# Optimization experiments

Measured on AMD Instinct MI355X. Metric: run time of the kernel, lower is better.

The kernel has to match this reference:

```python
import jax, jax.numpy as jnp
import numpy as np
import math

B, S, D, H, DFF, V = 8, 512, 512, 8, 2048, 32000
EPS = 1e-5

def _pe_table(max_len, d):
    pos = jnp.arange(max_len, dtype=jnp.float32)[:, None]
    i = jnp.arange(d)
    exponent = (2 * (i // 2)).astype(jnp.float32) / d
    angle = pos / jnp.power(10000.0, exponent)[None, :]
    return jnp.where(i % 2 == 0, jnp.sin(angle), jnp.cos(angle))

def _ln(x, g, b):
    mu = jnp.mean(x, -1, keepdims=True)
    var = jnp.mean((x - mu) ** 2, -1, keepdims=True)
    return g * (x - mu) * jax.lax.rsqrt(var + EPS) + b

def setup_inputs() -> dict:
    key = jax.random.key(0)
    ks = jax.random.split(key, 16)
    n = jax.random.normal
    return {
        "tokens": jax.random.randint(ks[0], (B, S), 0, V, dtype=jnp.int32),
        "emb": n(ks[1], (V, D), jnp.float32),
        "pe": _pe_table(1000, D),
        "Wq": n(ks[2], (H, D, D), jnp.float32), "bq": jnp.zeros((H, D), jnp.float32),
        "Wk": n(ks[3], (H, D, D), jnp.float32), "bk": jnp.zeros((H, D), jnp.float32),
        "Wv": n(ks[4], (H, D, D), jnp.float32), "bv": jnp.zeros((H, D), jnp.float32),
        "Wo": n(ks[5], (H * D, D), jnp.float32), "bo": jnp.zeros((D,), jnp.float32),
        "g1": jnp.ones((D,), jnp.float32), "be1": jnp.zeros((D,), jnp.float32),
        "W1": n(ks[6], (D, DFF), jnp.float32), "b1": jnp.zeros((DFF,), jnp.float32),
        "W2": n(ks[7], (DFF, D), jnp.float32), "b2": jnp.zeros((D,), jnp.float32),
        "g2": jnp.ones((D,), jnp.float32), "be2": jnp.zeros((D,), jnp.float32),
        "Wf": n(ks[8], (D, V), jnp.float32), "bf": jnp.zeros((V,), jnp.float32),
    }

def reference(tokens, emb, pe, Wq, bq, Wk, bk, Wv, bv, Wo, bo, g1, be1,
              W1, b1, W2, b2, g2, be2, Wf, bf):
    x = emb[tokens] + pe[:tokens.shape[1]]  # [B,S,D]
    res = x
    # input-level "causal" mask over (seq, feature) plane, as in the source
    mask = jnp.triu(jnp.ones((S, D), dtype=bool), k=1)
    xm = jnp.where(mask, 0.0, x)
    scale = 1.0 / math.sqrt(D)
    q = jnp.einsum('bsd,hde->hbse', xm, Wq) + bq[:, None, None, :]
    k = jnp.einsum('bsd,hde->hbse', xm, Wk) + bk[:, None, None, :]
    v = jnp.einsum('bsd,hde->hbse', xm, Wv) + bv[:, None, None, :]
    attn = jax.nn.softmax(jnp.einsum('hbse,hbte->hbst', q, k) * scale, axis=-1)
    o = jnp.einsum('hbst,hbte->hbse', attn, v)  # [H,B,S,D]
    cat = o.transpose(1, 2, 0, 3).reshape(B, S, H * D)  # matches torch.cat head order
    x = _ln(res + (cat @ Wo + bo), g1, be1)
    res = x
    ff = jax.nn.relu(x @ W1 + b1) @ W2 + b2
    x = _ln(res + ff, g2, be2)
    return x @ Wf + bf  # [B,S,V]
```

## Files before the change

### kernel.cpp

```cpp
#include <hip/hip_runtime.h>

typedef unsigned short u16;
typedef unsigned int u32;
typedef short s16x8 __attribute__((ext_vector_type(8)));
typedef __bf16 bf16x8 __attribute__((ext_vector_type(8)));
typedef float f32x4 __attribute__((ext_vector_type(4)));

#define DEVI static __device__ __forceinline__

#define SS 512
#define DD 512
#define NFF 2048
#define VV 32000
#define MTOT 4096
#define HD 4096
#define KC 1536

DEVI float bf2f(u16 h){ return __uint_as_float(((u32)h) << 16); }
DEVI u16 f2bf(float f){
  u32 u = __float_as_uint(f);
  return (u16)((u + 0x7FFFu + ((u >> 16) & 1u)) >> 16);
}
DEVI float ldf(const void* p, long i, int isbf){
  return isbf ? bf2f(((const u16*)p)[i]) : ((const float*)p)[i];
}

DEVI f32x4 mfma16(s16x8 a, s16x8 b, f32x4 c){
  return __builtin_amdgcn_mfma_f32_16x16x32_bf16(
      __builtin_bit_cast(bf16x8, a), __builtin_bit_cast(bf16x8, b), c, 0, 0, 0);
}

typedef const __attribute__((address_space(1))) unsigned int* gup;
typedef __attribute__((address_space(3))) unsigned int* lup;
DEVI void gload16(const void* g, void* l){
  __builtin_amdgcn_global_load_lds((gup)g, (lup)l, 16, 0, 0);
}

DEVI float wave_redsum(float v){
  #pragma unroll
  for (int off = 32; off > 0; off >>= 1) v += __shfl_xor(v, off, 64);
  return v;
}

__global__ void k_dflag(const void* pe, int* flag){
  flag[0] = (*(const u32*)pe == 0x3F800000u) ? 1 : 0;
}

__global__ __launch_bounds__(256) void k_embed(
    const int* __restrict__ tok, const void* __restrict__ emb, const void* __restrict__ pe,
    float* __restrict__ x, u16* __restrict__ xm2, const int* __restrict__ dflag)
{
  int isbf = dflag[0];
  int blk = blockIdx.x;
  int s = blk & (SS - 1);
  int t = tok[blk];
  long rb = (long)blk * 1024;
  for (int d = threadIdx.x; d < DD; d += 256){
    float e = ldf(emb, (long)t * DD + d, isbf) + ldf(pe, (long)s * DD + d, isbf);
    x[(long)blk * DD + d] = e;
    float m = (d <= s) ? e : 0.f;
    u16 hi = f2bf(m);
    u16 lo = f2bf(m - bf2f(hi));
    xm2[rb + d] = hi;
    xm2[rb + 512 + d] = lo;
  }
}

__global__ __launch_bounds__(256) void k_wsplitT(
    const void* __restrict__ Wq, const void* __restrict__ Wk,
    u16* __restrict__ Wq2, u16* __restrict__ Wk2, const int* __restrict__ dflag)
{
  int isbf = dflag[0];
  int zz = blockIdx.z;
  const void* in = (zz < 8) ? Wq : Wk;
  u16* out = (zz < 8) ? Wq2 : Wk2;
  int z = zz & 7;
  long zin = (long)z * DD * DD;
  long zout = (long)z * DD * 1024;
  __shared__ float t[32][33];
  int e0 = blockIdx.x * 32, d0 = blockIdx.y * 32;
  int tx = threadIdx.x & 31, ty = threadIdx.x >> 5;
  #pragma unroll
  for (int i = 0; i < 4; i++){
    int d = ty + i * 8;
    t[d][tx] = ldf(in, zin + (long)(d0 + d) * DD + e0 + tx, isbf);
  }
  __syncthreads();
  #pragma unroll
  for (int i = 0; i < 4; i++){
    int e = ty + i * 8;
    float v = t[tx][e];
    u16 hi = f2bf(v);
    u16 lo = f2bf(v - bf2f(hi));
    long ob = zout + (long)(e0 + e) * 1024 + d0 + tx;
    out[ob] = hi;
    out[ob + 512] = lo;
  }
}

__global__ __launch_bounds__(256) void k_transAll(
    const void* __restrict__ Wv, const void* __restrict__ Wo,
    const void* __restrict__ W1, const void* __restrict__ W2,
    const void* __restrict__ Wf,
    u16* __restrict__ WvT, u16* __restrict__ WoT, u16* __restrict__ W1T,
    u16* __restrict__ W2T, u16* __restrict__ WfT, const int* __restrict__ dflag)
{
  int isbf = dflag[0];
  int f = blockIdx.x;
  const void* in; u16* out; int R, C, gx, loc;
  if (f < 2048)      { in = Wv; out = WvT; R = 512;  C = 512;   gx = 16;   loc = f; }
  else if (f < 4096) { in = Wo; out = WoT; R = 4096; C = 512;   gx = 16;   loc = f - 2048; }
  else if (f < 5120) { in = W1; out = W1T; R = 512;  C = 2048;  gx = 64;   loc = f - 4096; }
  else if (f < 6144) { in = W2; out = W2T; R = 2048; C = 512;   gx = 16;   loc = f - 5120; }
  else               { in = Wf; out = WfT; R = 512;  C = 32000; gx = 1000; loc = f - 6144; }
  int bx = loc % gx;
  int rest = loc / gx;
  int gy = R >> 5;
  int by = rest % gy, z = rest / gy;
  long zo = (long)z * R * C;
  __shared__ float t[32][33];
  int c0 = bx * 32, r0 = by * 32;
  int tx = threadIdx.x & 31, ty = threadIdx.x >> 5;
  #pragma unroll
  for (int i = 0; i < 4; i++){
    int r = ty + i * 8;
    t[r][tx] = ldf(in, zo + (long)(r0 + r) * C + c0 + tx, isbf);
  }
  __syncthreads();
  #pragma unroll
  for (int i = 0; i < 4; i++){
    int c = ty + i * 8;
    out[zo + (long)(c0 + c) * R + r0 + tx] = f2bf(t[tx][c]);
  }
}

enum { EP_QK = 0, EP_SCALE = 1, EP_VT = 2, EP_CAT = 3, EP_OUT = 4,
       EP_F32RES = 5, EP_RELU = 6 };

template<int MODE, bool GSWAP>
__global__ __launch_bounds__(256) void k_mfma(
    const u16* __restrict__ A, long sA, int lda,
    const u16* __restrict__ Bt, long sB,
    void* __restrict__ Cv,
    const void* __restrict__ bias,
    const float* __restrict__ res,
    int K, int ldc, float scale,
    const int* __restrict__ dflag)
{
  int isbf = dflag[0];
  int z = blockIdx.z;
  const u16* Ab = A + (long)z * sA;
  const u16* Bb = Bt + (long)z * sB;
  __shared__ __align__(16) u16 As[2][4][128][8];
  __shared__ __align__(16) u16 Bs[2][4][128][8];
  int m0 = (GSWAP ? blockIdx.x : blockIdx.y) * 128;
  int n0 = (GSWAP ? blockIdx.y : blockIdx.x) * 128;
  int tid = threadIdx.x;
  int lane = tid & 63, w = tid >> 6;
  int wr = (w >> 1) * 64, wc = (w & 1) * 64;
  int l15 = lane & 15, l4 = lane >> 4;
  int s0 = w * 64 + lane;
  int ar0 = s0 & 127, ak0 = s0 >> 7;
  int ak1 = ak0 + 2;
  f32x4 zero = {0.f, 0.f, 0.f, 0.f};
  f32x4 acc[4][4];
  #pragma unroll
  for (int i = 0; i < 4; i++)
    #pragma unroll
    for (int j = 0; j < 4; j++) acc[i][j] = zero;

  const long arow0 = (long)(m0 + ar0) * lda;
  const long brow0 = (long)(n0 + ar0) * K;

  #define STAGE(buf, k0) do{ \
    u16* AsF = &As[buf][0][0][0]; \
    u16* BsF = &Bs[buf][0][0][0]; \
    gload16(Ab + arow0 + (k0) + ak0 * 8, AsF + (long)(w * 64) * 8); \
    gload16(Ab + arow0 + (k0) + ak1 * 8, AsF + (long)(256 + w * 64) * 8); \
    gload16(Bb + brow0 + (k0) + ak0 * 8, BsF + (long)(w * 64) * 8); \
    gload16(Bb + brow0 + (k0) + ak1 * 8, BsF + (long)(256 + w * 64) * 8); \
  }while(0)

  #define COMPUTE(buf) do{ \
    s16x8 af[4], bfr[4]; \
    _Pragma("unroll") \
    for (int i = 0; i < 4; i++) af[i] = *(const s16x8*)&As[buf][l4][wr + i * 16 + l15][0]; \
    _Pragma("unroll") \
    for (int j = 0; j < 4; j++) bfr[j] = *(const s16x8*)&Bs[buf][l4][wc + j * 16 + l15][0]; \
    _Pragma("unroll") \
    for (int i = 0; i < 4; i++) \
      _Pragma("unroll") \
      for (int j = 0; j < 4; j++) \
        acc[i][j] = mfma16(af[i], bfr[j], acc[i][j]); \
  }while(0)

  STAGE(0, 0);
  __syncthreads();
  for (int k0 = 0; k0 < K; k0 += 64){
    STAGE(1, k0 + 32);
    COMPUTE(0);
    __syncthreads();
    if (k0 + 64 < K) STAGE(0, k0 + 64);
    COMPUTE(1);
    __syncthreads();
  }
  #undef STAGE
  #undef COMPUTE

  int mbase = m0 + wr + l4 * 4;
  int nbase = n0 + wc + l15;
  if constexpr (MODE == EP_F32RES){
    float* C = (float*)Cv;
    #pragma unroll
    for (int j = 0; j < 4; j++){
      int n = nbase + j * 16;
      float badd = ldf(bias, n, isbf);
      #pragma unroll
      for (int i = 0; i < 4; i++)
        #pragma unroll
        for (int r = 0; r < 4; r++){
          long a = (long)(mbase + i * 16 + r) * ldc + n;
          C[a] = acc[i][j][r] + badd + res[a];
        }
    }
  } else if constexpr (MODE == EP_RELU){
    u16* C = (u16*)Cv;
    #pragma unroll
    for (int j = 0; j < 4; j++){
      int n = nbase + j * 16;
      float badd = ldf(bias, n, isbf);
      #pragma unroll
      for (int i = 0; i < 4; i++)
        #pragma unroll
        for (int r = 0; r < 4; r++)
          C[(long)(mbase + i * 16 + r) * ldc + n] = f2bf(fmaxf(acc[i][j][r] + badd, 0.f));
    }
  }
}

template<int MODE, bool GSWAP, int AMAP, int BMAP>
__global__ __launch_bounds__(512, 2) void k_mfma2(
    const u16* __restrict__ A, long sA, int lda,
    const u16* __restrict__ Bt, long sB, int ldb,
    void* __restrict__ Cv,
    const void* __restrict__ bias,
    const float* __restrict__ res,
    int K, int ldc, float scale,
    const int* __restrict__ dflag)
{
  int isbf = dflag[0];
  int z = blockIdx.z;
  const u16* Ab = A + (long)z * sA;
  const u16* Bb = Bt + (long)z * sB;
  __shared__ __align__(16) char smem[65536];
  u16* SA = (u16*)smem;
  u16* SB = (u16*)(smem + 32768);
  int m0 = (GSWAP ? blockIdx.x : blockIdx.y) * 256;
  int n0 = (GSWAP ? blockIdx.y : blockIdx.x) * 256;
  int tid = threadIdx.x;
  int lane = tid & 63, w = tid >> 6;
  int wm = (w >> 2) * 128, wn = (w & 3) * 64;
  int l15 = lane & 15, l4 = lane >> 4;
  int row = tid & 255, ob = tid >> 8;
  f32x4 zero = {0.f, 0.f, 0.f, 0.f};
  f32x4 acc[8][4];
  #pragma unroll
  for (int i = 0; i < 8; i++)
    #pragma unroll
    for (int j = 0; j < 4; j++) acc[i][j] = zero;

  const long arow0 = (long)(m0 + row) * lda;
  const long brow0 = (long)(n0 + row) * ldb;

  #define STAGE2(buf, k0_) do{ \
    int ka = (AMAP == 1) ? ((k0_) < 512 ? (k0_) : (k0_) - 512) \
           : (AMAP == 2) ? ((k0_) < 1024 ? (k0_) : (k0_) - 1024) : (k0_); \
    int kb = (BMAP == 1) ? ((k0_) < 512 ? (k0_) : (k0_) - 512) \
           : (BMAP == 2) ? ((k0_) < 1024 ? (k0_) : (k0_) - 1024) : (k0_); \
    gload16(Ab + arow0 + ka + ob * 8,       SA + ((buf) * 8192 + (ob * 256 + row) * 8)); \
    gload16(Ab + arow0 + ka + (ob + 2) * 8, SA + ((buf) * 8192 + ((ob + 2) * 256 + row) * 8)); \
    gload16(Bb + brow0 + kb + ob * 8,       SB + ((buf) * 8192 + (ob * 256 + row) * 8)); \
    gload16(Bb + brow0 + kb + (ob + 2) * 8, SB + ((buf) * 8192 + ((ob + 2) * 256 + row) * 8)); \
  }while(0)

  #define COMPUTE2(buf) do{ \
    s16x8 bfr[4]; \
    _Pragma("unroll") \
    for (int j = 0; j < 4; j++) \
      bfr[j] = *(const s16x8*)(SB + ((buf) * 8192 + l4 * 2048 + (wn + j * 16 + l15) * 8)); \
    _Pragma("unroll") \
    for (int i = 0; i < 8; i++){ \
      s16x8 af = *(const s16x8*)(SA + ((buf) * 8192 + l4 * 2048 + (wm + i * 16 + l15) * 8)); \
      _Pragma("unroll") \
      for (int j = 0; j < 4; j++) \
        acc[i][j] = mfma16(af, bfr[j], acc[i][j]); \
    } \
  }while(0)

  STAGE2(0, 0);
  __syncthreads();
  for (int k0 = 0; k0 < K; k0 += 64){
    STAGE2(1, k0 + 32);
    COMPUTE2(0);
    __syncthreads();
    if (k0 + 64 < K) STAGE2(0, k0 + 64);
    COMPUTE2(1);
    __syncthreads();
  }
  #undef STAGE2
  #undef COMPUTE2

  int mbase = m0 + wm + l4 * 4;
  int nbase = n0 + wn + l15;
  if constexpr (MODE == EP_CAT){
    u16* C = (u16*)Cv;
    int h = z >> 3, b = z & 7;
    #pragma unroll
    for (int i = 0; i < 8; i++){
      int s = mbase + i * 16;
      #pragma unroll
      for (int j = 0; j < 4; j++){
        int n = nbase + j * 16;
        #pragma unroll
        for (int r = 0; r < 4; r++)
          C[((long)b * SS + s + r) * HD + (long)h * DD + n] = f2bf(acc[i][j][r]);
      }
    }
  }
}

__global__ __launch_bounds__(512, 2) void k_out8(
    const u16* __restrict__ A, const u16* __restrict__ Bt,
    float* __restrict__ O, const void* __restrict__ bias,
    int NT, const int* __restrict__ dflag)
{
  int isbf = dflag[0];
  __shared__ __align__(16) char smem[131072];
  u16* SM = (u16*)smem;
  int f = blockIdx.x + gridDim.x * blockIdx.y;
  int qx = (gridDim.x * gridDim.y) >> 3;
  int L = (f & 7) * qx + (f >> 3);
  int m0 = (L % gridDim.x) * 256;
  int n0 = (L / gridDim.x) * 256;
  int tid = threadIdx.x;
  int lane = tid & 63, w = tid >> 6;
  int wm = (w >> 2) * 128, wn = (w & 3) * 64;
  int l15 = lane & 15, l4 = lane >> 4;
  f32x4 zero = {0.f, 0.f, 0.f, 0.f};
  f32x4 acc[8][4];
  #pragma unroll
  for (int i = 0; i < 8; i++)
    #pragma unroll
    for (int j = 0; j < 4; j++) acc[i][j] = zero;

  int rr = tid & 127, kc1 = tid >> 7;

  #define STAGEU(c, Tt, u) do{ \
    const u16* gb = (((u) & 1) == 0) ? A : Bt; \
    int base0 = (((u) & 1) == 0) ? m0 : n0; \
    int r2 = ((u) >> 1) * 128 + rr; \
    long gsrc = (long)(base0 + r2) * 512 + (Tt) * 64; \
    u16* lb = SM + (c) * 32768 + ((((u) & 1) == 0) ? 0 : 16384); \
    gload16(gb + gsrc + kc1 * 8,       lb + (kc1 * 256 + r2) * 8); \
    gload16(gb + gsrc + (kc1 + 4) * 8, lb + ((kc1 + 4) * 256 + r2) * 8); \
  }while(0)

  STAGEU(0, 0, 0); STAGEU(0, 0, 1); STAGEU(0, 0, 2); STAGEU(0, 0, 3);

  int cur = 0;
  for (int T = 0; T < NT; T++){
    int nxt = cur ^ 1;
    int more = (T + 1 < NT);
    s16x8 af[8];
    #pragma unroll
    for (int q = 0; q < 4; q++){
      if (more) STAGEU(nxt, T + 1, q);
      if (q == 0){
        if (more) asm volatile("s_waitcnt vmcnt(2)" ::: "memory");
        else      asm volatile("s_waitcnt vmcnt(0)" ::: "memory");
      }
      __builtin_amdgcn_s_barrier();
      __builtin_amdgcn_sched_barrier(0);
      int ks = q >> 1, jh = q & 1;
      if (jh == 0){
        #pragma unroll
        for (int i = 0; i < 8; i++)
          af[i] = *(const s16x8*)(SM + cur * 32768 +
                    ((ks * 4 + l4) * 256 + (wm + i * 16 + l15)) * 8);
      }
      s16x8 b0 = *(const s16x8*)(SM + cur * 32768 + 16384 +
                    ((ks * 4 + l4) * 256 + (wn + (jh * 2) * 16 + l15)) * 8);
      s16x8 b1 = *(const s16x8*)(SM + cur * 32768 + 16384 +
                    ((ks * 4 + l4) * 256 + (wn + (jh * 2 + 1) * 16 + l15)) * 8);
      __builtin_amdgcn_s_setprio(1);
      #pragma unroll
      for (int i = 0; i < 8; i++){
        acc[i][jh * 2]     = mfma16(af[i], b0, acc[i][jh * 2]);
        acc[i][jh * 2 + 1] = mfma16(af[i], b1, acc[i][jh * 2 + 1]);
      }
      __builtin_amdgcn_s_setprio(0);
    }
    __builtin_amdgcn_s_barrier();
    __builtin_amdgcn_sched_barrier(0);
    cur = nxt;
  }
  #undef STAGEU

  float* ldsT = (float*)smem;
  const int RST = 260;
  int hs16 = (w >> 2) * 16;
  float badd[4];
  #pragma unroll
  for (int j = 0; j < 4; j++) badd[j] = ldf(bias, n0 + wn + j * 16 + l15, isbf);
  #pragma unroll
  for (int i = 0; i < 8; i++){
    __syncthreads();
    #pragma unroll
    for (int j = 0; j < 4; j++){
      int col = wn + j * 16 + l15;
      #pragma unroll
      for (int r = 0; r < 4; r++)
        ldsT[(hs16 + l4 * 4 + r) * RST + col] = acc[i][j][r] + badd[j];
    }
    __syncthreads();
    #pragma unroll
    for (int p = 0; p < 4; p++){
      int chunk = tid + p * 512;
      int lr = chunk >> 6, c4 = chunk & 63;
      int gm = m0 + (lr >> 4) * 128 + i * 16 + (lr & 15);
      f32x4 v = *(f32x4*)&ldsT[lr * RST + c4 * 4];
      __builtin_nontemporal_store(v, (f32x4*)&O[(long)gm * VV + n0 + c4 * 4]);
    }
  }
}

__global__ __launch_bounds__(512, 2) void k_proj8(
    const u16* __restrict__ xm2,
    const u16* __restrict__ Wq2, const u16* __restrict__ Wk2, const u16* __restrict__ WvT,
    u16* __restrict__ q2, u16* __restrict__ k2, u16* __restrict__ vT,
    const void* __restrict__ bq, const void* __restrict__ bk, const void* __restrict__ bv,
    const int* __restrict__ dflag)
{
  int isbf = dflag[0];
  int zz = blockIdx.z;
  int z, ldb, NT, mode;
  const u16* Bb; const void* bias; u16* C;
  if (zz < 16){
    mode = 0; z = zz & 7;
    Bb = (zz < 8 ? Wq2 : Wk2) + (long)z * 524288;
    ldb = 1024; NT = 24;
    bias = (zz < 8) ? bq : bk;
    C = (zz < 8) ? q2 : k2;
  } else {
    mode = 1; z = zz - 16;
    Bb = WvT + (long)z * 262144;
    ldb = 512; NT = 8;
    bias = bv;
    C = vT;
  }
  const u16* Ab = xm2;
  __shared__ __align__(16) char smem[131072];
  u16* SM = (u16*)smem;
  int m0 = blockIdx.y * 256;
  int n0 = blockIdx.x * 256;
  int tid = threadIdx.x;
  int lane = tid & 63, w = tid >> 6;
  int wm = (w >> 2) * 128, wn = (w & 3) * 64;
  int l15 = lane & 15, l4 = lane >> 4;
  f32x4 zero = {0.f, 0.f, 0.f, 0.f};
  f32x4 acc[8][4];
  #pragma unroll
  for (int i = 0; i < 8; i++)
    #pragma unroll
    for (int j = 0; j < 4; j++) acc[i][j] = zero;

  int rr = tid & 127, kc1 = tid >> 7;

  #define KA8(Tt) (mode == 0 ? (((Tt) * 64 < 512) ? (Tt) * 64 : (Tt) * 64 - 512) : (Tt) * 64)
  #define KB8(Tt) (mode == 0 ? (((Tt) * 64 < 1024) ? (Tt) * 64 : (Tt) * 64 - 1024) : (Tt) * 64)

  #define STAGEU(c, Tt, u) do{ \
    const u16* gb = (((u) & 1) == 0) ? Ab : Bb; \
    long rs = (((u) & 1) == 0) ? 1024 : (long)ldb; \
    int base0 = (((u) & 1) == 0) ? m0 : n0; \
    int tk = (((u) & 1) == 0) ? KA8(Tt) : KB8(Tt); \
    int r2 = ((u) >> 1) * 128 + rr; \
    long gsrc = (long)(base0 + r2) * rs + tk; \
    u16* lb = SM + (c) * 32768 + ((((u) & 1) == 0) ? 0 : 16384); \
    gload16(gb + gsrc + kc1 * 8,       lb + (kc1 * 256 + r2) * 8); \
    gload16(gb + gsrc + (kc1 + 4) * 8, lb + ((kc1 + 4) * 256 + r2) * 8); \
  }while(0)

  STAGEU(0, 0, 0); STAGEU(0, 0, 1); STAGEU(0, 0, 2); STAGEU(0, 0, 3);

  int cur = 0;
  for (int T = 0; T < NT; T++){
    int nxt = cur ^ 1;
    int more = (T + 1 < NT);
    s16x8 af[8];
    #pragma unroll
    for (int q = 0; q < 4; q++){
      if (more) STAGEU(nxt, T + 1, q);
      if (q == 0){
        if (more) asm volatile("s_waitcnt vmcnt(2)" ::: "memory");
        else      asm volatile("s_waitcnt vmcnt(0)" ::: "memory");
      }
      __builtin_amdgcn_s_barrier();
      __builtin_amdgcn_sched_barrier(0);
      int ks = q >> 1, jh = q & 1;
      if (jh == 0){
        #pragma unroll
        for (int i = 0; i < 8; i++)
          af[i] = *(const s16x8*)(SM + cur * 32768 +
                    ((ks * 4 + l4) * 256 + (wm + i * 16 + l15)) * 8);
      }
      s16x8 b0 = *(const s16x8*)(SM + cur * 32768 + 16384 +
                    ((ks * 4 + l4) * 256 + (wn + (jh * 2) * 16 + l15)) * 8);
      s16x8 b1 = *(const s16x8*)(SM + cur * 32768 + 16384 +
                    ((ks * 4 + l4) * 256 + (wn + (jh * 2 + 1) * 16 + l15)) * 8);
      __builtin_amdgcn_s_setprio(1);
      #pragma unroll
      for (int i = 0; i < 8; i++){
        acc[i][jh * 2]     = mfma16(af[i], b0, acc[i][jh * 2]);
        acc[i][jh * 2 + 1] = mfma16(af[i], b1, acc[i][jh * 2 + 1]);
      }
      __builtin_amdgcn_s_setprio(0);
    }
    __builtin_amdgcn_s_barrier();
    __builtin_amdgcn_sched_barrier(0);
    cur = nxt;
  }
  #undef STAGEU
  #undef KA8
  #undef KB8

  int mbase = m0 + wm + l4 * 4;
  int nbase = n0 + wn + l15;
  if (mode == 0){
    u16* Cz = C + (long)z * ((long)MTOT * 1024);
    #pragma unroll
    for (int j = 0; j < 4; j++){
      int n = nbase + j * 16;
      float badd = ldf(bias, (long)z * DD + n, isbf);
      #pragma unroll
      for (int i = 0; i < 8; i++)
        #pragma unroll
        for (int r = 0; r < 4; r++){
          float qv = acc[i][j][r] + badd;
          u16 hi = f2bf(qv);
          u16 lo = f2bf(qv - bf2f(hi));
          long rb = (long)(mbase + i * 16 + r) * 1024;
          Cz[rb + n] = hi;
          Cz[rb + 512 + n] = lo;
        }
    }
  } else {
    #pragma unroll
    for (int i = 0; i < 8; i++){
      int mrow = mbase + i * 16;
      int b = mrow >> 9, s = mrow & (SS - 1);
      #pragma unroll
      for (int j = 0; j < 4; j++){
        int n = nbase + j * 16;
        float badd = ldf(bias, (long)z * DD + n, isbf);
        ushort4 pk;
        pk.x = f2bf(acc[i][j][0] + badd); pk.y = f2bf(acc[i][j][1] + badd);
        pk.z = f2bf(acc[i][j][2] + badd); pk.w = f2bf(acc[i][j][3] + badd);
        *(ushort4*)&C[((long)(z * 8 + b) * DD + n) * SS + s] = pk;
      }
    }
  }
}

template<int AMAP, int BMAP>
__global__ __launch_bounds__(512, 2) void k_fsm(
    const u16* __restrict__ A, long sA, int lda,
    const u16* __restrict__ Bt, long sB, int ldb,
    u16* __restrict__ P, int K, float scale,
    const int* __restrict__ dflag)
{
  int z = blockIdx.z;
  const u16* Ab = A + (long)z * sA;
  const u16* Bb = Bt + (long)z * sB;
  __shared__ __align__(16) char smem[81920];
  u16* SA = (u16*)smem;
  u16* SB = (u16*)(smem + 16384);
  int m0 = blockIdx.x * 128;
  int tid = threadIdx.x;
  int lane = tid & 63, w = tid >> 6;
  int wn = w * 64;
  int l15 = lane & 15, l4 = lane >> 4;
  f32x4 zero = {0.f, 0.f, 0.f, 0.f};
  f32x4 acc[8][4];
  #pragma unroll
  for (int i = 0; i < 8; i++)
    #pragma unroll
    for (int j = 0; j < 4; j++) acc[i][j] = zero;

  const long arow0 = (long)(m0 + (tid & 127)) * lda;
  const int akc = tid >> 7;
  const long brow0 = (long)tid * ldb;

  #define STAGEF(buf, k0_) do{ \
    int ka = (AMAP == 1) ? ((k0_) < 512 ? (k0_) : (k0_) - 512) \
           : (AMAP == 2) ? ((k0_) < 1024 ? (k0_) : (k0_) - 1024) : (k0_); \
    int kb = (BMAP == 1) ? ((k0_) < 512 ? (k0_) : (k0_) - 512) \
           : (BMAP == 2) ? ((k0_) < 1024 ? (k0_) : (k0_) - 1024) : (k0_); \
    gload16(Ab + arow0 + ka + akc * 8, SA + ((buf) * 4096 + tid * 8)); \
    gload16(Bb + brow0 + kb + 0,  SB + ((buf) * 16384 + (0 * 512 + tid) * 8)); \
    gload16(Bb + brow0 + kb + 8,  SB + ((buf) * 16384 + (1 * 512 + tid) * 8)); \
    gload16(Bb + brow0 + kb + 16, SB + ((buf) * 16384 + (2 * 512 + tid) * 8)); \
    gload16(Bb + brow0 + kb + 24, SB + ((buf) * 16384 + (3 * 512 + tid) * 8)); \
  }while(0)

  #define COMPUTEF(buf) do{ \
    s16x8 bfr[4]; \
    _Pragma("unroll") \
    for (int j = 0; j < 4; j++) \
      bfr[j] = *(const s16x8*)(SB + ((buf) * 16384 + l4 * 4096 + (wn + j * 16 + l15) * 8)); \
    _Pragma("unroll") \
    for (int i = 0; i < 8; i++){ \
      s16x8 af = *(const s16x8*)(SA + ((buf) * 4096 + l4 * 1024 + (i * 16 + l15) * 8)); \
      _Pragma("unroll") \
      for (int j = 0; j < 4; j++) \
        acc[i][j] = mfma16(af, bfr[j], acc[i][j]); \
    } \
  }while(0)

  STAGEF(0, 0);
  __syncthreads();
  for (int k0 = 0; k0 < K; k0 += 64){
    STAGEF(1, k0 + 32);
    COMPUTEF(0);
    __syncthreads();
    if (k0 + 64 < K) STAGEF(0, k0 + 64);
    COMPUTEF(1);
    __syncthreads();
  }
  #undef STAGEF
  #undef COMPUTEF

  float* sred = (float*)smem;
  float* srow = (float*)(smem + 4096);

  #pragma unroll
  for (int i = 0; i < 8; i++)
    #pragma unroll
    for (int j = 0; j < 4; j++)
      acc[i][j] *= scale;

  #pragma unroll
  for (int i = 0; i < 8; i++)
    #pragma unroll
    for (int r = 0; r < 4; r++){
      float m = fmaxf(fmaxf(acc[i][0][r], acc[i][1][r]),
                      fmaxf(acc[i][2][r], acc[i][3][r]));
      #pragma unroll
      for (int off = 1; off < 16; off <<= 1) m = fmaxf(m, __shfl_xor(m, off, 64));
      if (l15 == 0) sred[w * 128 + l4 * 4 + i * 16 + r] = m;
    }
  __syncthreads();
  if (tid < 128){
    float m = sred[tid];
    #pragma unroll
    for (int w2 = 1; w2 < 8; w2++) m = fmaxf(m, sred[w2 * 128 + tid]);
    srow[tid] = m;
  }
  __syncthreads();
  #pragma unroll
  for (int i = 0; i < 8; i++)
    #pragma unroll
    for (int r = 0; r < 4; r++){
      float rm = srow[l4 * 4 + i * 16 + r];
      float s = 0.f;
      #pragma unroll
      for (int j = 0; j < 4; j++){
        float e = expf(acc[i][j][r] - rm);
        acc[i][j][r] = e;
        s += e;
      }
      #pragma unroll
      for (int off = 1; off < 16; off <<= 1) s += __shfl_xor(s, off, 64);
      if (l15 == 0) sred[w * 128 + l4 * 4 + i * 16 + r] = s;
    }
  __syncthreads();
  if (tid < 128){
    float s = 0.f;
    #pragma unroll
    for (int w2 = 0; w2 < 8; w2++) s += sred[w2 * 128 + tid];
    srow[tid] = 1.f / s;
  }
  __syncthreads();
  u16* Pz = P + (long)z * ((long)SS * SS);
  u16* pb = (u16*)(smem + 8192);
  const int PST = 520;
  #pragma unroll
  for (int ii = 0; ii < 4; ii++){
    __syncthreads();
    #pragma unroll
    for (int s2 = 0; s2 < 2; s2++){
      int i = ii * 2 + s2;
      #pragma unroll
      for (int r = 0; r < 4; r++){
        int rl = l4 * 4 + i * 16 + r;
        float inv = srow[rl];
        #pragma unroll
        for (int j = 0; j < 4; j++)
          pb[(s2 * 16 + l4 * 4 + r) * PST + wn + j * 16 + l15] = f2bf(acc[i][j][r] * inv);
      }
    }
    __syncthreads();
    #pragma unroll
    for (int p = 0; p < 8; p++){
      int chunk = tid + p * 512;
      int lr = chunk >> 7, c8 = chunk & 127;
      ushort4 v = *(ushort4*)&pb[lr * PST + c8 * 4];
      *(ushort4*)&Pz[(long)(m0 + ii * 32 + lr) * SS + c8 * 4] = v;
    }
  }
}

template<bool WF32>
__global__ __launch_bounds__(256) void k_ln(
    const float* __restrict__ X, const void* __restrict__ g, const void* __restrict__ be,
    u16* __restrict__ Yb, float* __restrict__ Yf, const int* __restrict__ dflag)
{
  int isbf = dflag[0];
  int row = blockIdx.x * 4 + (threadIdx.x >> 6);
  int lane = threadIdx.x & 63;
  const float* p = X + (long)row * DD + lane * 8;
  float4 v0 = *(const float4*)p;
  float4 v1 = *(const float4*)(p + 4);
  float v[8] = {v0.x, v0.y, v0.z, v0.w, v1.x, v1.y, v1.z, v1.w};
  float s = 0.f;
  #pragma unroll
  for (int i = 0; i < 8; i++) s += v[i];
  s = wave_redsum(s);
  float mu = s * (1.f / DD);
  float d_[8], sq = 0.f;
  #pragma unroll
  for (int i = 0; i < 8; i++){ d_[i] = v[i] - mu; sq += d_[i] * d_[i]; }
  sq = wave_redsum(sq);
  float rs = 1.f / sqrtf(sq * (1.f / DD) + 1e-5f);
  #pragma unroll
  for (int i = 0; i < 8; i++){
    int dd = lane * 8 + i;
    float y = ldf(g, dd, isbf) * d_[i] * rs + ldf(be, dd, isbf);
    Yb[(long)row * DD + dd] = f2bf(y);
    if (WF32) Yf[(long)row * DD + dd] = y;
  }
}

extern "C" void kernel_launch(void* const* d_in, const int* in_sizes, int n_in,
                              void* d_out, int out_size, void* d_ws, size_t ws_size,
                              hipStream_t stream)
{
  const int* tokens = (const int*)d_in[0];
  const void* emb = d_in[1];
  const void* pe  = d_in[2];
  const void* Wq  = d_in[3];
  const void* bq  = d_in[4];
  const void* Wk  = d_in[5];
  const void* bk  = d_in[6];
  const void* Wv  = d_in[7];
  const void* bv  = d_in[8];
  const void* Wo  = d_in[9];
  const void* bo  = d_in[10];
  const void* g1  = d_in[11];
  const void* be1 = d_in[12];
  const void* W1  = d_in[13];
  const void* b1  = d_in[14];
  const void* W2  = d_in[15];
  const void* b2  = d_in[16];
  const void* g2  = d_in[17];
  const void* be2 = d_in[18];
  const void* Wf  = d_in[19];
  const void* bfb = d_in[20];
  float* out = (float*)d_out;
  char* ws = (char*)d_ws;
  char* DO = (char*)d_out;

  const size_t MB = 1ull << 20;
  int* dflag = (int*)ws;
  u16* x2b   = (u16*)(ws + 1 * MB);
  u16* WfT   = (u16*)(ws + 8 * MB);

  float* x    = (float*)(DO + 0 * MB);
  u16*   xm2  = (u16*)(DO + 8 * MB);
  u16*   Wq2  = (u16*)(DO + 16 * MB);
  u16*   Wk2  = (u16*)(DO + 24 * MB);
  u16*   WvT  = (u16*)(DO + 32 * MB);
  u16*   WoT  = (u16*)(DO + 36 * MB);
  u16*   W1T  = (u16*)(DO + 40 * MB);
  u16*   W2T  = (u16*)(DO + 42 * MB);
  u16*   q2   = (u16*)(DO + 48 * MB);
  u16*   k2   = (u16*)(DO + 112 * MB);
  u16*   attn = (u16*)(DO + 240 * MB);
  u16*   vT   = (u16*)(DO + 272 * MB);
  u16*   cat  = (u16*)(DO + 304 * MB);
  float* proj = (float*)(DO + 336 * MB);
  float* x1f  = (float*)(DO + 344 * MB);
  u16*   x1b  = (u16*)(DO + 352 * MB);
  u16*   ff1  = (u16*)(DO + 356 * MB);
  float* ff2  = (float*)(DO + 372 * MB);

  const float scale = 0.04419417382415922f;
  const long HSL = 262144;
  const long QSL = 524288;

  k_dflag<<<1, 1, 0, stream>>>(pe, dflag);
  k_embed<<<dim3(4096), 256, 0, stream>>>(tokens, emb, pe, x, xm2, dflag);

  k_wsplitT<<<dim3(16, 16, 16), 256, 0, stream>>>(Wq, Wk, Wq2, Wk2, dflag);
  k_transAll<<<dim3(22144), 256, 0, stream>>>(
      Wv, Wo, W1, W2, Wf, WvT, WoT, W1T, W2T, WfT, dflag);

  k_proj8<<<dim3(2, 16, 24), 512, 0, stream>>>(
      xm2, Wq2, Wk2, WvT, q2, k2, vT, bq, bk, bv, dflag);

  k_fsm<1, 2><<<dim3(4, 1, 64), 512, 0, stream>>>(
      q2, QSL, 1024, k2, QSL, 1024, attn, KC, scale, dflag);

  k_mfma2<EP_CAT, false, 0, 0><<<dim3(2, 2, 64), 512, 0, stream>>>(
      attn, HSL, SS, vT, HSL, 512, cat, nullptr, nullptr, SS, 0, 0.f, dflag);

  k_mfma<EP_F32RES, false><<<dim3(4, 32, 1), 256, 0, stream>>>(
      cat, 0, HD, WoT, 0, proj, bo, x, HD, DD, 0.f, dflag);
  k_ln<true><<<dim3(1024), 256, 0, stream>>>(proj, g1, be1, x1b, x1f, dflag);

  k_mfma<EP_RELU, false><<<dim3(16, 32, 1), 256, 0, stream>>>(
      x1b, 0, DD, W1T, 0, ff1, b1, nullptr, DD, NFF, 0.f, dflag);
  k_mfma<EP_F32RES, false><<<dim3(4, 32, 1), 256, 0, stream>>>(
      ff1, 0, NFF, W2T, 0, ff2, b2, x1f, NFF, DD, 0.f, dflag);
  k_ln<false><<<dim3(1024), 256, 0, stream>>>(ff2, g2, be2, x2b, nullptr, dflag);

  k_out8<<<dim3(16, 125, 1), 512, 0, stream>>>(x2b, WfT, out, bfb, 8, dflag);
}
```

Baseline: 929.5 us.

## Replace attn·V kernel with a deeper-pipelined 64-wide-K GEMM using split barriers

The generic k_mfma2 used for attn@V is replaced by a dedicated k_cat8 kernel. It stages 64-wide K tiles into a 128KB double buffer in four sub-loads interleaved with compute. It uses explicit vmcnt waits, raw s_barrier plus sched_barrier, and s_setprio around the MFMA bursts. The aim is better overlap of global loads with MFMA work and fewer full syncthreads per K step. The larger LDS footprint may limit occupancy, and the hand-tuned waitcnt ordering is fragile.

```diff
diff --git a/kernel.cpp b/kernel.cpp
--- a/kernel.cpp
+++ b/kernel.cpp
@@ -134,8 +134,7 @@
   }
 }
 
-enum { EP_QK = 0, EP_SCALE = 1, EP_VT = 2, EP_CAT = 3, EP_OUT = 4,
-       EP_F32RES = 5, EP_RELU = 6 };
+enum { EP_F32RES = 5, EP_RELU = 6 };
 
 template<int MODE, bool GSWAP>
 __global__ __launch_bounds__(256) void k_mfma(
@@ -238,97 +237,6 @@
   }
 }
 
-template<int MODE, bool GSWAP, int AMAP, int BMAP>
-__global__ __launch_bounds__(512, 2) void k_mfma2(
-    const u16* __restrict__ A, long sA, int lda,
-    const u16* __restrict__ Bt, long sB, int ldb,
-    void* __restrict__ Cv,
-    const void* __restrict__ bias,
-    const float* __restrict__ res,
-    int K, int ldc, float scale,
-    const int* __restrict__ dflag)
-{
-  int isbf = dflag[0];
-  int z = blockIdx.z;
-  const u16* Ab = A + (long)z * sA;
-  const u16* Bb = Bt + (long)z * sB;
-  __shared__ __align__(16) char smem[65536];
-  u16* SA = (u16*)smem;
-  u16* SB = (u16*)(smem + 32768);
-  int m0 = (GSWAP ? blockIdx.x : blockIdx.y) * 256;
-  int n0 = (GSWAP ? blockIdx.y : blockIdx.x) * 256;
-  int tid = threadIdx.x;
-  int lane = tid & 63, w = tid >> 6;
-  int wm = (w >> 2) * 128, wn = (w & 3) * 64;
-  int l15 = lane & 15, l4 = lane >> 4;
-  int row = tid & 255, ob = tid >> 8;
-  f32x4 zero = {0.f, 0.f, 0.f, 0.f};
-  f32x4 acc[8][4];
-  #pragma unroll
-  for (int i = 0; i < 8; i++)
-    #pragma unroll
-    for (int j = 0; j < 4; j++) acc[i][j] = zero;
-
-  const long arow0 = (long)(m0 + row) * lda;
-  const long brow0 = (long)(n0 + row) * ldb;
-
-  #define STAGE2(buf, k0_) do{ \
-    int ka = (AMAP == 1) ? ((k0_) < 512 ? (k0_) : (k0_) - 512) \
-           : (AMAP == 2) ? ((k0_) < 1024 ? (k0_) : (k0_) - 1024) : (k0_); \
-    int kb = (BMAP == 1) ? ((k0_) < 512 ? (k0_) : (k0_) - 512) \
-           : (BMAP == 2) ? ((k0_) < 1024 ? (k0_) : (k0_) - 1024) : (k0_); \
-    gload16(Ab + arow0 + ka + ob * 8,       SA + ((buf) * 8192 + (ob * 256 + row) * 8)); \
-    gload16(Ab + arow0 + ka + (ob + 2) * 8, SA + ((buf) * 8192 + ((ob + 2) * 256 + row) * 8)); \
-    gload16(Bb + brow0 + kb + ob * 8,       SB + ((buf) * 8192 + (ob * 256 + row) * 8)); \
-    gload16(Bb + brow0 + kb + (ob + 2) * 8, SB + ((buf) * 8192 + ((ob + 2) * 256 + row) * 8)); \
-  }while(0)
-
-  #define COMPUTE2(buf) do{ \
-    s16x8 bfr[4]; \
-    _Pragma("unroll") \
-    for (int j = 0; j < 4; j++) \
-      bfr[j] = *(const s16x8*)(SB + ((buf) * 8192 + l4 * 2048 + (wn + j * 16 + l15) * 8)); \
-    _Pragma("unroll") \
-    for (int i = 0; i < 8; i++){ \
-      s16x8 af = *(const s16x8*)(SA + ((buf) * 8192 + l4 * 2048 + (wm + i * 16 + l15) * 8)); \
-      _Pragma("unroll") \
-      for (int j = 0; j < 4; j++) \
-        acc[i][j] = mfma16(af, bfr[j], acc[i][j]); \
-    } \
-  }while(0)
-
-  STAGE2(0, 0);
-  __syncthreads();
-  for (int k0 = 0; k0 < K; k0 += 64){
-    STAGE2(1, k0 + 32);
-    COMPUTE2(0);
-    __syncthreads();
-    if (k0 + 64 < K) STAGE2(0, k0 + 64);
-    COMPUTE2(1);
-    __syncthreads();
-  }
-  #undef STAGE2
-  #undef COMPUTE2
-
-  int mbase = m0 + wm + l4 * 4;
-  int nbase = n0 + wn + l15;
-  if constexpr (MODE == EP_CAT){
-    u16* C = (u16*)Cv;
-    int h = z >> 3, b = z & 7;
-    #pragma unroll
-    for (int i = 0; i < 8; i++){
-      int s = mbase + i * 16;
-      #pragma unroll
-      for (int j = 0; j < 4; j++){
-        int n = nbase + j * 16;
-        #pragma unroll
-        for (int r = 0; r < 4; r++)
-          C[((long)b * SS + s + r) * HD + (long)h * DD + n] = f2bf(acc[i][j][r]);
-      }
-    }
-  }
-}
-
 __global__ __launch_bounds__(512, 2) void k_out8(
     const u16* __restrict__ A, const u16* __restrict__ Bt,
     float* __restrict__ O, const void* __restrict__ bias,
@@ -568,6 +476,97 @@
         pk.z = f2bf(acc[i][j][2] + badd); pk.w = f2bf(acc[i][j][3] + badd);
         *(ushort4*)&C[((long)(z * 8 + b) * DD + n) * SS + s] = pk;
       }
+    }
+  }
+}
+
+__global__ __launch_bounds__(512, 2) void k_cat8(
+    const u16* __restrict__ attn, const u16* __restrict__ vT,
+    u16* __restrict__ cat, const int* __restrict__ dflag)
+{
+  int z = blockIdx.z;
+  const u16* Ab = attn + (long)z * 262144;
+  const u16* Bb = vT + (long)z * 262144;
+  __shared__ __align__(16) char smem[131072];
+  u16* SM = (u16*)smem;
+  int m0 = blockIdx.y * 256;
+  int n0 = blockIdx.x * 256;
+  int tid = threadIdx.x;
+  int lane = tid & 63, w = tid >> 6;
+  int wm = (w >> 2) * 128, wn = (w & 3) * 64;
+  int l15 = lane & 15, l4 = lane >> 4;
+  f32x4 zero = {0.f, 0.f, 0.f, 0.f};
+  f32x4 acc[8][4];
+  #pragma unroll
+  for (int i = 0; i < 8; i++)
+    #pragma unroll
+    for (int j = 0; j < 4; j++) acc[i][j] = zero;
+
+  int rr = tid & 127, kc1 = tid >> 7;
+
+  #define STAGEU(c, Tt, u) do{ \
+    const u16* gb = (((u) & 1) == 0) ? Ab : Bb; \
+    int base0 = (((u) & 1) == 0) ? m0 : n0; \
+    int r2 = ((u) >> 1) * 128 + rr; \
+    long gsrc = (long)(base0 + r2) * 512 + (Tt) * 64; \
+    u16* lb = SM + (c) * 32768 + ((((u) & 1) == 0) ? 0 : 16384); \
+    gload16(gb + gsrc + kc1 * 8,       lb + (kc1 * 256 + r2) * 8); \
+    gload16(gb + gsrc + (kc1 + 4) * 8, lb + ((kc1 + 4) * 256 + r2) * 8); \
+  }while(0)
+
+  STAGEU(0, 0, 0); STAGEU(0, 0, 1); STAGEU(0, 0, 2); STAGEU(0, 0, 3);
+
+  int cur = 0;
+  for (int T = 0; T < 8; T++){
+    int nxt = cur ^ 1;
+    int more = (T + 1 < 8);
+    s16x8 af[8];
+    #pragma unroll
+    for (int q = 0; q < 4; q++){
+      if (more) STAGEU(nxt, T + 1, q);
+      if (q == 0){
+        if (more) asm volatile("s_waitcnt vmcnt(2)" ::: "memory");
+        else      asm volatile("s_waitcnt vmcnt(0)" ::: "memory");
+      }
+      __builtin_amdgcn_s_barrier();
+      __builtin_amdgcn_sched_barrier(0);
+      int ks = q >> 1, jh = q & 1;
+      if (jh == 0){
+        #pragma unroll
+        for (int i = 0; i < 8; i++)
+          af[i] = *(const s16x8*)(SM + cur * 32768 +
+                    ((ks * 4 + l4) * 256 + (wm + i * 16 + l15)) * 8);
+      }
+      s16x8 b0 = *(const s16x8*)(SM + cur * 32768 + 16384 +
+                    ((ks * 4 + l4) * 256 + (wn + (jh * 2) * 16 + l15)) * 8);
+      s16x8 b1 = *(const s16x8*)(SM + cur * 32768 + 16384 +
+                    ((ks * 4 + l4) * 256 + (wn + (jh * 2 + 1) * 16 + l15)) * 8);
+      __builtin_amdgcn_s_setprio(1);
+      #pragma unroll
+      for (int i = 0; i < 8; i++){
+        acc[i][jh * 2]     = mfma16(af[i], b0, acc[i][jh * 2]);
+        acc[i][jh * 2 + 1] = mfma16(af[i], b1, acc[i][jh * 2 + 1]);
+      }
+      __builtin_amdgcn_s_setprio(0);
+    }
+    __builtin_amdgcn_s_barrier();
+    __builtin_amdgcn_sched_barrier(0);
+    cur = nxt;
+  }
+  #undef STAGEU
+
+  int mbase = m0 + wm + l4 * 4;
+  int nbase = n0 + wn + l15;
+  int h = z >> 3, b = z & 7;
+  #pragma unroll
+  for (int i = 0; i < 8; i++){
+    int s = mbase + i * 16;
+    #pragma unroll
+    for (int j = 0; j < 4; j++){
+      int n = nbase + j * 16;
+      #pragma unroll
+      for (int r = 0; r < 4; r++)
+        cat[((long)b * SS + s + r) * HD + (long)h * DD + n] = f2bf(acc[i][j][r]);
     }
   }
 }
@@ -805,7 +804,6 @@
   float* ff2  = (float*)(DO + 372 * MB);
 
   const float scale = 0.04419417382415922f;
-  const long HSL = 262144;
   const long QSL = 524288;
 
   k_dflag<<<1, 1, 0, stream>>>(pe, dflag);
@@ -821,8 +819,7 @@
   k_fsm<1, 2><<<dim3(4, 1, 64), 512, 0, stream>>>(
       q2, QSL, 1024, k2, QSL, 1024, attn, KC, scale, dflag);
 
-  k_mfma2<EP_CAT, false, 0, 0><<<dim3(2, 2, 64), 512, 0, stream>>>(
-      attn, HSL, SS, vT, HSL, 512, cat, nullptr, nullptr, SS, 0, 0.f, dflag);
+  k_cat8<<<dim3(2, 2, 64), 512, 0, stream>>>(attn, vT, cat, dflag);
 
   k_mfma<EP_F32RES, false><<<dim3(4, 32, 1), 256, 0, stream>>>(
       cat, 0, HD, WoT, 0, proj, bo, x, HD, DD, 0.f, dflag);
```

New measurement: 924.3 us. About the same (-0.6%).
